# Performance work log

Hardware: AMD Instinct MI355X
Metric: run time of the kernel (lower is better)

## Reference

```python
import jax, jax.numpy as jnp
import numpy as np

SIZE = 384  # output resolution
SCALE = (0.8, 1.0)


def _bilinear_crop_resize(img, cs, top, left):
    """img: [C,H,W]; cs/top/left: int32 scalars. Crop [top:top+cs, left:left+cs],
    resize to SIZE x SIZE with bilinear, align_corners=False (PyTorch semantics)."""
    csf = cs.astype(jnp.float32)
    # source coords within the crop, clamped like PyTorch (src = max(src,0), upper bounded)
    coords = (jnp.arange(SIZE, dtype=jnp.float32) + 0.5) * (csf / SIZE) - 0.5
    coords = jnp.clip(coords, 0.0, csf - 1.0)
    i0 = jnp.floor(coords).astype(jnp.int32)
    i1 = jnp.minimum(i0 + 1, cs - 1)
    w = coords - i0.astype(jnp.float32)  # [SIZE]
    y0, y1 = i0 + top, i1 + top
    x0, x1 = i0 + left, i1 + left
    wy, wx = w[:, None], w[None, :]
    g = lambda yy, xx: img[:, yy[:, None], xx[None, :]]  # [C,SIZE,SIZE]
    return (g(y0, x0) * (1 - wy) * (1 - wx)
            + g(y0, x1) * (1 - wy) * wx
            + g(y1, x0) * wy * (1 - wx)
            + g(y1, x1) * wy * wx)


def _nearest_crop_resize(msk, cs, top, left):
    """msk: [1,H,W]. PyTorch mode='nearest': src_idx = floor(dst * in/out)."""
    idx = jnp.floor(jnp.arange(SIZE, dtype=jnp.float32) * cs.astype(jnp.float32) / SIZE).astype(jnp.int32)
    idx = jnp.minimum(idx, cs - 1)
    y, x = idx + top, idx + left
    return msk[:, y[:, None], x[None, :]]


def setup_inputs() -> dict:
    key = jax.random.key(0)
    k1, k2, k3, k4, k5 = jax.random.split(key, 5)
    B, C, H, W = 32, 3, 512, 512
    image = jax.random.normal(k1, (B, C, H, W), dtype=jnp.float32)
    mask = (jax.random.uniform(k2, (B, 1, H, W)) > 0.5).astype(jnp.float32)
    scale = jax.random.uniform(k3, (B,), minval=SCALE[0], maxval=SCALE[1])
    crop_size = (scale * min(H, W)).astype(jnp.int32)
    max_y = (H - crop_size).astype(jnp.float32)
    max_x = (W - crop_size).astype(jnp.float32)
    top = jnp.where(max_y > 0, jnp.floor(jax.random.uniform(k4, (B,)) * max_y), 0.0).astype(jnp.int32)
    left = jnp.where(max_x > 0, jnp.floor(jax.random.uniform(k5, (B,)) * max_x), 0.0).astype(jnp.int32)
    return {"image": image, "mask": mask, "crop_size": crop_size, "top": top, "left": left}


def reference(image, mask, crop_size, top, left):
    img_out = jax.vmap(_bilinear_crop_resize)(image, crop_size, top, left)
    msk_out = jax.vmap(_nearest_crop_resize)(mask, crop_size, top, left)
    return img_out, msk_out
```

## Files before the change

### kernel.cpp

```cpp
#include <hip/hip_runtime.h>


constexpr int OUT = 384;
constexpr int H = 512;
constexpr int W = 512;
constexpr int B = 32;
constexpr int C = 3;
constexpr int RPB = 4;
constexpr int GPB = OUT / RPB;
constexpr int NBLK = B * GPB;
constexpr int BPX  = NBLK / 8;
constexpr int NSLOT = 6;
constexpr int LROWS = C * NSLOT;
constexpr int LDSW  = 520;

typedef float f32x4 __attribute__((ext_vector_type(4)));

__global__ __launch_bounds__(OUT) void rrc_pair_kernel(
    const float* __restrict__ image,
    const float* __restrict__ mask,
    const int* __restrict__ crop_size,
    const int* __restrict__ top,
    const int* __restrict__ left,
    float* __restrict__ img_out,
    float* __restrict__ msk_out)
{
    __shared__ float lds[LROWS * LDSW];

    const int hw = blockIdx.x;
    const int logical = (hw & 7) * BPX + (hw >> 3);
    const int b  = logical / GPB;
    const int i0 = (logical % GPB) * RPB;
    const int tid = (int)threadIdx.x;

    const int cs = crop_size[b];
    const int t  = top[b];
    const int l  = left[b];
    const float csf = (float)cs;
    const float s   = csf / (float)OUT;

    float cy0 = ((float)i0 + 0.5f) * s - 0.5f;
    cy0 = fminf(fmaxf(cy0, 0.0f), csf - 1.0f);
    const int base_y = (int)floorf(cy0);

    const float* imgb = image + (size_t)b * C * H * W;

    #pragma unroll
    for (int k = 0; k < 6; ++k) {
        const int q   = tid + k * OUT;
        const int r   = q >> 7;
        const int col = (q & 127) * 4;
        const int c    = r / NSLOT;
        const int slot = r % NSLOT;
        const int y = min(t + base_y + slot, H - 1);
        const float* src = imgb + ((size_t)c * H + (size_t)y) * W + col;
        f32x4 v = *(const f32x4*)src;
        *(f32x4*)&lds[r * LDSW + col] = v;
        if ((q & 127) == 127) lds[r * LDSW + 512] = v[3];
    }

    float cx = ((float)tid + 0.5f) * s - 0.5f;
    cx = fminf(fmaxf(cx, 0.0f), csf - 1.0f);
    const int   ix0 = (int)floorf(cx);
    const float wx  = cx - (float)ix0;
    const int   x0  = ix0 + l;

    const int mx = min((tid * cs) / OUT, cs - 1) + l;

    float mval[RPB];
    #pragma unroll
    for (int r4 = 0; r4 < RPB; ++r4) {
        const int i = i0 + r4;
        int my = min((i * cs) / OUT, cs - 1);
        mval[r4] = mask[((size_t)b * H + (size_t)(my + t)) * W + mx];
    }

    __syncthreads();

    #pragma unroll
    for (int r4 = 0; r4 < RPB; ++r4) {
        const int i = i0 + r4;
        float cy = ((float)i + 0.5f) * s - 0.5f;
        cy = fminf(fmaxf(cy, 0.0f), csf - 1.0f);
        int   iy0 = (int)floorf(cy);
        int   iy1 = min(iy0 + 1, cs - 1);
        float wy  = cy - (float)iy0;
        const int slot0 = iy0 - base_y;
        const int slot1 = min(iy1 - base_y, NSLOT - 1);

        const float w00 = (1.0f - wy) * (1.0f - wx);
        const float w01 = (1.0f - wy) * wx;
        const float w10 = wy * (1.0f - wx);
        const float w11 = wy * wx;

        const size_t o_base = (size_t)b * C * OUT * OUT + (size_t)i * OUT + (size_t)tid;

        #pragma unroll
        for (int c = 0; c < C; ++c) {
            const float* rA = &lds[(c * NSLOT + slot0) * LDSW + x0];
            const float* rB = &lds[(c * NSLOT + slot1) * LDSW + x0];
            float v00 = rA[0], v01 = rA[1];
            float v10 = rB[0], v11 = rB[1];
            float rr = v00 * w00 + v01 * w01 + v10 * w10 + v11 * w11;
            __builtin_nontemporal_store(rr, img_out + o_base + (size_t)c * OUT * OUT);
        }
        __builtin_nontemporal_store(mval[r4],
            msk_out + (size_t)b * OUT * OUT + (size_t)i * OUT + (size_t)tid);
    }
}

extern "C" void kernel_launch(void* const* d_in, const int* in_sizes, int n_in,
                              void* d_out, int out_size, void* d_ws, size_t ws_size,
                              hipStream_t stream) {
    const float* image = (const float*)d_in[0];
    const float* mask  = (const float*)d_in[1];
    const int* cs      = (const int*)d_in[2];
    const int* top     = (const int*)d_in[3];
    const int* left    = (const int*)d_in[4];

    float* img_out = (float*)d_out;
    float* msk_out = img_out + (size_t)B * C * OUT * OUT;

    dim3 block(OUT);
    dim3 grid(NBLK);
    hipLaunchKernelGGL(rrc_pair_kernel, grid, block, 0, stream,
                       image, mask, cs, top, left, img_out, msk_out);
}
```

Before: 32.99 us.

## Process six row groups per block with double-buffered LDS prefetch

Each block now handles six 4-row output groups instead of one, cutting the grid to one sixth. Global loads for the next group's source rows go into registers while the current group is interpolated, then are written to the other LDS buffer. This aims to hide global load latency and amortize per-block setup. The cost is doubled LDS use (about 72KB), fewer and longer blocks, and a barrier per group, which may reduce occupancy and parallelism on a GPU with many CUs.

```diff
diff --git a/kernel.cpp b/kernel.cpp
--- a/kernel.cpp
+++ b/kernel.cpp
@@ -8,15 +8,17 @@
 constexpr int C = 3;
 constexpr int RPB = 4;
 constexpr int GPB = OUT / RPB;
-constexpr int NBLK = B * GPB;
+constexpr int GRP_PER_BLK = 6;
+constexpr int BLK_PER_IMG = GPB / GRP_PER_BLK;
+constexpr int NBLK = B * BLK_PER_IMG;
 constexpr int BPX  = NBLK / 8;
 constexpr int NSLOT = 6;
 constexpr int LROWS = C * NSLOT;
-constexpr int LDSW  = 520;
+constexpr int BUFSZ = LROWS * W;
 
 typedef float f32x4 __attribute__((ext_vector_type(4)));
 
-__global__ __launch_bounds__(OUT) void rrc_pair_kernel(
+__global__ __launch_bounds__(OUT, 3) void rrc_pair_kernel(
     const float* __restrict__ image,
     const float* __restrict__ mask,
     const int* __restrict__ crop_size,
@@ -25,12 +27,12 @@
     float* __restrict__ img_out,
     float* __restrict__ msk_out)
 {
-    __shared__ float lds[LROWS * LDSW];
+    __shared__ float lds[2 * BUFSZ + 8];
 
     const int hw = blockIdx.x;
     const int logical = (hw & 7) * BPX + (hw >> 3);
-    const int b  = logical / GPB;
-    const int i0 = (logical % GPB) * RPB;
+    const int b  = logical / BLK_PER_IMG;
+    const int g0 = (logical % BLK_PER_IMG) * GRP_PER_BLK;
     const int tid = (int)threadIdx.x;
 
     const int cs = crop_size[b];
@@ -39,24 +41,18 @@
     const float csf = (float)cs;
     const float s   = csf / (float)OUT;
 
-    float cy0 = ((float)i0 + 0.5f) * s - 0.5f;
-    cy0 = fminf(fmaxf(cy0, 0.0f), csf - 1.0f);
-    const int base_y = (int)floorf(cy0);
+    const float* imgb = image + (size_t)b * C * H * W;
+    const float* mskb = mask + (size_t)b * H * W;
 
-    const float* imgb = image + (size_t)b * C * H * W;
-
+    int ck[6], slotk[6], colk[6], qd[6];
     #pragma unroll
     for (int k = 0; k < 6; ++k) {
-        const int q   = tid + k * OUT;
-        const int r   = q >> 7;
-        const int col = (q & 127) * 4;
-        const int c    = r / NSLOT;
-        const int slot = r % NSLOT;
-        const int y = min(t + base_y + slot, H - 1);
-        const float* src = imgb + ((size_t)c * H + (size_t)y) * W + col;
-        f32x4 v = *(const f32x4*)src;
-        *(f32x4*)&lds[r * LDSW + col] = v;
-        if ((q & 127) == 127) lds[r * LDSW + 512] = v[3];
+        const int q = tid + k * OUT;
+        const int r = q >> 7;
+        colk[k]  = (q & 127) * 4;
+        ck[k]    = r / NSLOT;
+        slotk[k] = r % NSLOT;
+        qd[k]    = q * 4;
     }
 
     float cx = ((float)tid + 0.5f) * s - 0.5f;
@@ -64,48 +60,91 @@
     const int   ix0 = (int)floorf(cx);
     const float wx  = cx - (float)ix0;
     const int   x0  = ix0 + l;
+    const int   mx  = min((tid * cs) / OUT, cs - 1) + l;
 
-    const int mx = min((tid * cs) / OUT, cs - 1) + l;
+    auto base_y_of = [&](int grp) -> int {
+        float cy0 = ((float)(grp * RPB) + 0.5f) * s - 0.5f;
+        cy0 = fminf(fmaxf(cy0, 0.0f), csf - 1.0f);
+        return (int)floorf(cy0);
+    };
 
-    float mval[RPB];
-    #pragma unroll
-    for (int r4 = 0; r4 < RPB; ++r4) {
-        const int i = i0 + r4;
-        int my = min((i * cs) / OUT, cs - 1);
-        mval[r4] = mask[((size_t)b * H + (size_t)(my + t)) * W + mx];
+    int cur_base_y = base_y_of(g0);
+    {
+        f32x4 v[6];
+        #pragma unroll
+        for (int k = 0; k < 6; ++k) {
+            const int y = min(t + cur_base_y + slotk[k], H - 1);
+            v[k] = *(const f32x4*)(imgb + ((size_t)ck[k] * H + (size_t)y) * W + colk[k]);
+        }
+        if (tid < 8) lds[2 * BUFSZ + tid] = 0.0f;
+        #pragma unroll
+        for (int k = 0; k < 6; ++k)
+            *(f32x4*)&lds[qd[k]] = v[k];
     }
-
     __syncthreads();
 
-    #pragma unroll
-    for (int r4 = 0; r4 < RPB; ++r4) {
-        const int i = i0 + r4;
-        float cy = ((float)i + 0.5f) * s - 0.5f;
-        cy = fminf(fmaxf(cy, 0.0f), csf - 1.0f);
-        int   iy0 = (int)floorf(cy);
-        int   iy1 = min(iy0 + 1, cs - 1);
-        float wy  = cy - (float)iy0;
-        const int slot0 = iy0 - base_y;
-        const int slot1 = min(iy1 - base_y, NSLOT - 1);
+    for (int gg = 0; gg < GRP_PER_BLK; ++gg) {
+        const int cur = gg & 1;
+        const int i0 = (g0 + gg) * RPB;
 
-        const float w00 = (1.0f - wy) * (1.0f - wx);
-        const float w01 = (1.0f - wy) * wx;
-        const float w10 = wy * (1.0f - wx);
-        const float w11 = wy * wx;
+        f32x4 nv[6];
+        int nbase_y = cur_base_y;
+        if (gg + 1 < GRP_PER_BLK) {
+            nbase_y = base_y_of(g0 + gg + 1);
+            #pragma unroll
+            for (int k = 0; k < 6; ++k) {
+                const int y = min(t + nbase_y + slotk[k], H - 1);
+                nv[k] = *(const f32x4*)(imgb + ((size_t)ck[k] * H + (size_t)y) * W + colk[k]);
+            }
+        }
 
-        const size_t o_base = (size_t)b * C * OUT * OUT + (size_t)i * OUT + (size_t)tid;
+        float mval[RPB];
+        #pragma unroll
+        for (int r4 = 0; r4 < RPB; ++r4) {
+            int my = min(((i0 + r4) * cs) / OUT, cs - 1);
+            mval[r4] = mskb[(size_t)(my + t) * W + mx];
+        }
 
+        const float* buf = &lds[cur * BUFSZ];
         #pragma unroll
-        for (int c = 0; c < C; ++c) {
-            const float* rA = &lds[(c * NSLOT + slot0) * LDSW + x0];
-            const float* rB = &lds[(c * NSLOT + slot1) * LDSW + x0];
-            float v00 = rA[0], v01 = rA[1];
-            float v10 = rB[0], v11 = rB[1];
-            float rr = v00 * w00 + v01 * w01 + v10 * w10 + v11 * w11;
-            __builtin_nontemporal_store(rr, img_out + o_base + (size_t)c * OUT * OUT);
+        for (int r4 = 0; r4 < RPB; ++r4) {
+            const int i = i0 + r4;
+            float cy = ((float)i + 0.5f) * s - 0.5f;
+            cy = fminf(fmaxf(cy, 0.0f), csf - 1.0f);
+            int   iy0 = (int)floorf(cy);
+            int   iy1 = min(iy0 + 1, cs - 1);
+            float wy  = cy - (float)iy0;
+            const int slot0 = iy0 - cur_base_y;
+            const int slot1 = min(iy1 - cur_base_y, NSLOT - 1);
+
+            const float w00 = (1.0f - wy) * (1.0f - wx);
+            const float w01 = (1.0f - wy) * wx;
+            const float w10 = wy * (1.0f - wx);
+            const float w11 = wy * wx;
+
+            const size_t o_base = (size_t)b * C * OUT * OUT + (size_t)i * OUT + (size_t)tid;
+
+            #pragma unroll
+            for (int c = 0; c < C; ++c) {
+                const float* rA = &buf[(c * NSLOT + slot0) * W];
+                const float* rB = &buf[(c * NSLOT + slot1) * W];
+                float v00 = rA[x0], v01 = rA[x0 + 1];
+                float v10 = rB[x0], v11 = rB[x0 + 1];
+                float rr = v00 * w00 + v01 * w01 + v10 * w10 + v11 * w11;
+                __builtin_nontemporal_store(rr, img_out + o_base + (size_t)c * OUT * OUT);
+            }
+            __builtin_nontemporal_store(mval[r4],
+                msk_out + (size_t)b * OUT * OUT + (size_t)i * OUT + (size_t)tid);
         }
-        __builtin_nontemporal_store(mval[r4],
-            msk_out + (size_t)b * OUT * OUT + (size_t)i * OUT + (size_t)tid);
+
+        if (gg + 1 < GRP_PER_BLK) {
+            float* nbuf = &lds[(cur ^ 1) * BUFSZ];
+            #pragma unroll
+            for (int k = 0; k < 6; ++k)
+                *(f32x4*)&nbuf[qd[k]] = nv[k];
+            cur_base_y = nbase_y;
+        }
+        __syncthreads();
     }
 }
 
```

Measured after the change: 34.93 us. +5.9%, slower.
